# Optimization experiments

Measured on AMD Instinct MI355X. Metric: run time of the kernel, lower is better.

## Reference

```python
import jax, jax.numpy as jnp
import numpy as np

RANK = 16
ALPHA = 16.0
IN_F = 4096
OUT_F = 11008
TOKENS = 64


def setup_inputs() -> dict:
    key = jax.random.key(0)
    k_x, k_w, k_s, k_a, k_b, k_bias = jax.random.split(key, 6)
    return {
        "x": jax.random.normal(k_x, (TOKENS, IN_F), dtype=jnp.float32),
        "weight_int4": jax.random.normal(k_w, (OUT_F, IN_F), dtype=jnp.float32),
        "weight_scale": jax.random.uniform(k_s, (OUT_F,), dtype=jnp.float32),
        "lora_A": jax.random.normal(k_a, (RANK, IN_F), dtype=jnp.float32) * 0.01,
        "lora_B": jax.random.normal(k_b, (OUT_F, RANK), dtype=jnp.float32),
        "bias": jax.random.normal(k_bias, (OUT_F,), dtype=jnp.float32),
    }


def reference(x, weight_int4, weight_scale, lora_A, lora_B, bias):
    # Dequantize: per-output-channel scale.  [out, in]
    weight = weight_int4 * weight_scale[:, None]
    # LoRA delta: B @ A scaled by alpha/rank.  [out, in]
    lora_weight = (lora_B @ lora_A) * (ALPHA / RANK)
    effective_weight = weight + lora_weight
    # F.linear: x @ W^T + b  ->  [tokens, out]
    return x @ effective_weight.T + bias
```

## Files before the change

### kernel.cpp

```cpp
#include <hip/hip_runtime.h>
#include <hip/hip_bf16.h>
#include <cstdint>

#define TOK   64
#define INF   4096
#define OUTF  11008
#define KCHUNKS 128
#define QCNT  8
#define NCHB  172

using bf16x8  = __attribute__((ext_vector_type(8))) __bf16;
using floatx4 = __attribute__((ext_vector_type(4))) float;

union B8u { uint32_t u[4]; uint4 q; bf16x8 v; };

__device__ __forceinline__ uint32_t hi2(float a, float b) {
    return (__float_as_uint(a) >> 16) | (__float_as_uint(b) & 0xffff0000u);
}
__device__ __forceinline__ float losub(float x) {
    return x - __uint_as_float(__float_as_uint(x) & 0xffff0000u);
}
__device__ __forceinline__ void packW(float4 a, float4 b, B8u& wh, B8u& wl) {
    wh.u[0] = hi2(a.x, a.y);  wh.u[1] = hi2(a.z, a.w);
    wh.u[2] = hi2(b.x, b.y);  wh.u[3] = hi2(b.z, b.w);
    wl.u[0] = hi2(losub(a.x), losub(a.y));
    wl.u[1] = hi2(losub(a.z), losub(a.w));
    wl.u[2] = hi2(losub(b.x), losub(b.y));
    wl.u[3] = hi2(losub(b.z), losub(b.w));
}

__global__ __launch_bounds__(256) void k_prep(const float* __restrict__ x,
        const float* __restrict__ A,
        unsigned short* __restrict__ xh, unsigned short* __restrict__ xl,
        float* __restrict__ tm) {
    int b = blockIdx.x;
    if (b < 1024) {
        int idx  = b * 256 + threadIdx.x;
        int j    = idx & 7;
        int lane = (idx >> 3) & 63;
        int kc   = (idx >> 9) & 127;
        int mt   = idx >> 16;
        int row  = mt * 16 + (lane & 15);
        int col  = kc * 32 + ((lane >> 4) << 3) + j;
        float v  = x[(size_t)row * INF + col];
        float lo = losub(v);
        xh[idx] = (unsigned short)(__float_as_uint(v) >> 16);
        xl[idx] = (unsigned short)(__float_as_uint(lo) >> 16);
    } else {
        int bb   = b - 1024;
        int t    = bb & 63;
        int wv   = threadIdx.x >> 6, lane = threadIdx.x & 63;
        int r    = (bb >> 6) * 4 + wv;
        const float4* xr = (const float4*)(x + (size_t)t * INF);
        const float4* ar = (const float4*)(A + (size_t)r * INF);
        float s = 0.f;
#pragma unroll
        for (int i = 0; i < INF / 4 / 64; ++i) {
            float4 a = xr[lane + i * 64], c = ar[lane + i * 64];
            s += a.x * c.x + a.y * c.y + a.z * c.z + a.w * c.w;
        }
#pragma unroll
        for (int off = 32; off > 0; off >>= 1) s += __shfl_down(s, off);
        if (lane == 0) tm[t * 16 + r] = s;
    }
}

template<bool ATOMIC>
__global__ __launch_bounds__(256, 2) void k_main(const float* __restrict__ W,
        const uint4* __restrict__ xh, const uint4* __restrict__ xl,
        const float* __restrict__ scale, float* __restrict__ part,
        float* __restrict__ out) {
    __shared__ uint4 wlds[2][1024];
    __shared__ uint4 xsl [2][1024];

    int tid  = threadIdx.x;
    int lane = tid & 63;
    int wv   = tid >> 6;
    int quad = lane >> 4;
    int nb   = blockIdx.x % NCHB;
    int q    = blockIdx.x / NCHB;
    int chl  = wv * 16 + (lane & 15);
    int ch   = nb * 64 + chl;

    const int kbase = q * 512;
    int rr = lane >> 4;
    int gg = lane & 15;

    floatx4 acc[4] = {};

    auto stage = [&](int p, int bsel) {
#pragma unroll
        for (int t = 0; t < 4; ++t) {
            int i = wv * 4 + t;
            int r = i * 4 + rr;
            int f = (gg - r) & 15;
            const float* src = W + (size_t)(nb * 64 + r) * INF
                             + kbase + p * 64 + f * 4;
            __builtin_amdgcn_global_load_lds(
                (const __attribute__((address_space(1))) uint32_t*)src,
                (__attribute__((address_space(3))) uint32_t*)&wlds[bsel][i * 64],
                16, 0, 0);
        }
#pragma unroll
        for (int t = 0; t < 4; ++t) {
            int j  = wv * 4 + t;
            int hl = j >> 3, mt = (j >> 1) & 3, kc = j & 1;
            const uint4* src = (hl ? xl : xh)
                + ((size_t)(mt * KCHUNKS + q * 16 + p * 2 + kc) * 64 + lane);
            __builtin_amdgcn_global_load_lds(
                (const __attribute__((address_space(1))) uint32_t*)src,
                (__attribute__((address_space(3))) uint32_t*)&xsl[bsel][j * 64],
                16, 0, 0);
        }
    };

    stage(0, 0);
    int cur = 0;
#pragma unroll
    for (int p = 0; p < 8; ++p) {
        __syncthreads();
        if (p < 7) stage(p + 1, cur ^ 1);

#pragma unroll
        for (int kc = 0; kc < 2; ++kc) {
            int f0 = kc * 8 + quad * 2;
            uint4 wf0 = wlds[cur][chl * 16 + ((f0     + chl) & 15)];
            uint4 wf1 = wlds[cur][chl * 16 + ((f0 + 1 + chl) & 15)];
            B8u wh, wl;
            packW(*(float4*)&wf0, *(float4*)&wf1, wh, wl);
#pragma unroll
            for (int mt = 0; mt < 4; ++mt) {
                B8u ah, al;
                ah.q = xsl[cur][(    mt * 2 + kc) * 64 + lane];
                al.q = xsl[cur][(8 + mt * 2 + kc) * 64 + lane];
                acc[mt] = __builtin_amdgcn_mfma_f32_16x16x32_bf16(ah.v, wh.v, acc[mt], 0, 0, 0);
                acc[mt] = __builtin_amdgcn_mfma_f32_16x16x32_bf16(ah.v, wl.v, acc[mt], 0, 0, 0);
                acc[mt] = __builtin_amdgcn_mfma_f32_16x16x32_bf16(al.v, wh.v, acc[mt], 0, 0, 0);
            }
        }
        cur ^= 1;
    }

#pragma unroll
    for (int mt = 0; mt < 4; ++mt) {
        int token = mt * 16 + quad * 4;
#pragma unroll
        for (int r = 0; r < 4; ++r) {
            if constexpr (ATOMIC) {
                atomicAdd(&out[(size_t)(token + r) * OUTF + ch], scale[ch] * acc[mt][r]);
            } else {
                part[((size_t)q * TOK + token + r) * OUTF + ch] = acc[mt][r];
            }
        }
    }
}

__global__ __launch_bounds__(256) void k_post(const float* __restrict__ part,
        const float* __restrict__ scale, const float* __restrict__ bias,
        const float* __restrict__ lB, const float* __restrict__ tm,
        float* __restrict__ out) {
    int o = blockIdx.x * 256 + threadIdx.x;
    int t = blockIdx.y;
    if (o >= OUTF) return;
    float s = 0.f;
#pragma unroll
    for (int qq = 0; qq < QCNT; ++qq)
        s += part[((size_t)qq * TOK + t) * OUTF + o];
    const float4* Br = (const float4*)(lB + (size_t)o * 16);
    const float4* tr = (const float4*)(tm + (size_t)t * 16);
    float l = 0.f;
#pragma unroll
    for (int i = 0; i < 4; ++i) {
        float4 b = Br[i], tt = tr[i];
        l += b.x * tt.x + b.y * tt.y + b.z * tt.z + b.w * tt.w;
    }
    out[(size_t)t * OUTF + o] = s * scale[o] + l + bias[o];
}

__global__ __launch_bounds__(256) void k_pre(const float* __restrict__ bias,
        const float* __restrict__ lB, const float* __restrict__ tm,
        float* __restrict__ out) {
    int o = blockIdx.x * 256 + threadIdx.x;
    int t = blockIdx.y;
    if (o >= OUTF) return;
    const float4* Br = (const float4*)(lB + (size_t)o * 16);
    const float4* tr = (const float4*)(tm + (size_t)t * 16);
    float l = 0.f;
#pragma unroll
    for (int i = 0; i < 4; ++i) {
        float4 b = Br[i], tt = tr[i];
        l += b.x * tt.x + b.y * tt.y + b.z * tt.z + b.w * tt.w;
    }
    out[(size_t)t * OUTF + o] = l + bias[o];
}

extern "C" void kernel_launch(void* const* d_in, const int* in_sizes, int n_in,
                              void* d_out, int out_size, void* d_ws, size_t ws_size,
                              hipStream_t stream) {
    const float* x     = (const float*)d_in[0];
    const float* W     = (const float*)d_in[1];
    const float* scale = (const float*)d_in[2];
    const float* lA    = (const float*)d_in[3];
    const float* lB    = (const float*)d_in[4];
    const float* bias  = (const float*)d_in[5];
    float* out = (float*)d_out;

    char* ws = (char*)d_ws;
    unsigned short* xh = (unsigned short*)(ws);
    unsigned short* xl = (unsigned short*)(ws + 524288);
    float* tm   = (float*)(ws + 1048576);
    float* part = (float*)(ws + 1052672);
    const size_t need = 1052672 + (size_t)QCNT * TOK * OUTF * 4;

    k_prep<<<1280, 256, 0, stream>>>(x, lA, xh, xl, tm);

    if (ws_size >= need) {
        k_main<false><<<NCHB * QCNT, 256, 0, stream>>>(W, (const uint4*)xh,
                (const uint4*)xl, scale, part, out);
        k_post<<<dim3(43, TOK), 256, 0, stream>>>(part, scale, bias, lB, tm, out);
    } else {
        k_pre<<<dim3(43, TOK), 256, 0, stream>>>(bias, lB, tm, out);
        k_main<true><<<NCHB * QCNT, 256, 0, stream>>>(W, (const uint4*)xh,
                (const uint4*)xl, scale, nullptr, out);
    }
}
```

Measured before the change: 280.8 us.

## Deepen K-loop pipeline to a 4-stage LDS ring with explicit vmcnt waits

Replaces the two-buffer, 64-wide K staging with a four-buffer ring of 32-wide K slices, keeping three stages of global-to-LDS loads in flight. Each iteration waits on vmcnt only for the oldest stage and then uses a raw s_barrier instead of __syncthreads. The goal is to hide more of the global-memory latency of streaming the fp32 weights. Total LDS use is unchanged. The trade-offs are smaller tiles, more barriers per block and hand-tuned waitcnt values that depend on how many loads each stage issues.

```diff
diff --git a/kernel.cpp b/kernel.cpp
--- a/kernel.cpp
+++ b/kernel.cpp
@@ -70,8 +70,8 @@
         const uint4* __restrict__ xh, const uint4* __restrict__ xl,
         const float* __restrict__ scale, float* __restrict__ part,
         float* __restrict__ out) {
-    __shared__ uint4 wlds[2][1024];
-    __shared__ uint4 xsl [2][1024];
+    __shared__ uint4 wlds[4][512];
+    __shared__ uint4 xsl [4][512];
 
     int tid  = threadIdx.x;
     int lane = tid & 63;
@@ -83,30 +83,30 @@
     int ch   = nb * 64 + chl;
 
     const int kbase = q * 512;
-    int rr = lane >> 4;
-    int gg = lane & 15;
+    int rsub = lane >> 3;
+    int gg   = lane & 7;
 
     floatx4 acc[4] = {};
 
     auto stage = [&](int p, int bsel) {
 #pragma unroll
-        for (int t = 0; t < 4; ++t) {
-            int i = wv * 4 + t;
-            int r = i * 4 + rr;
-            int f = (gg - r) & 15;
+        for (int t = 0; t < 2; ++t) {
+            int i = wv * 2 + t;
+            int r = i * 8 + rsub;
+            int f = (gg - r) & 7;
             const float* src = W + (size_t)(nb * 64 + r) * INF
-                             + kbase + p * 64 + f * 4;
+                             + kbase + p * 32 + f * 4;
             __builtin_amdgcn_global_load_lds(
                 (const __attribute__((address_space(1))) uint32_t*)src,
                 (__attribute__((address_space(3))) uint32_t*)&wlds[bsel][i * 64],
                 16, 0, 0);
         }
 #pragma unroll
-        for (int t = 0; t < 4; ++t) {
-            int j  = wv * 4 + t;
-            int hl = j >> 3, mt = (j >> 1) & 3, kc = j & 1;
+        for (int t = 0; t < 2; ++t) {
+            int j  = wv * 2 + t;
+            int hl = j >> 2, mt = j & 3;
             const uint4* src = (hl ? xl : xh)
-                + ((size_t)(mt * KCHUNKS + q * 16 + p * 2 + kc) * 64 + lane);
+                + ((size_t)(mt * KCHUNKS + q * 16 + p) * 64 + lane);
             __builtin_amdgcn_global_load_lds(
                 (const __attribute__((address_space(1))) uint32_t*)src,
                 (__attribute__((address_space(3))) uint32_t*)&xsl[bsel][j * 64],
@@ -115,30 +115,31 @@
     };
 
     stage(0, 0);
-    int cur = 0;
-#pragma unroll
-    for (int p = 0; p < 8; ++p) {
-        __syncthreads();
-        if (p < 7) stage(p + 1, cur ^ 1);
-
-#pragma unroll
-        for (int kc = 0; kc < 2; ++kc) {
-            int f0 = kc * 8 + quad * 2;
-            uint4 wf0 = wlds[cur][chl * 16 + ((f0     + chl) & 15)];
-            uint4 wf1 = wlds[cur][chl * 16 + ((f0 + 1 + chl) & 15)];
-            B8u wh, wl;
-            packW(*(float4*)&wf0, *(float4*)&wf1, wh, wl);
-#pragma unroll
-            for (int mt = 0; mt < 4; ++mt) {
-                B8u ah, al;
-                ah.q = xsl[cur][(    mt * 2 + kc) * 64 + lane];
-                al.q = xsl[cur][(8 + mt * 2 + kc) * 64 + lane];
-                acc[mt] = __builtin_amdgcn_mfma_f32_16x16x32_bf16(ah.v, wh.v, acc[mt], 0, 0, 0);
-                acc[mt] = __builtin_amdgcn_mfma_f32_16x16x32_bf16(ah.v, wl.v, acc[mt], 0, 0, 0);
-                acc[mt] = __builtin_amdgcn_mfma_f32_16x16x32_bf16(al.v, wh.v, acc[mt], 0, 0, 0);
-            }
-        }
-        cur ^= 1;
+    stage(1, 1);
+    stage(2, 2);
+
+#pragma unroll
+    for (int p = 0; p < 16; ++p) {
+        if (p < 14)       asm volatile("s_waitcnt vmcnt(8)" ::: "memory");
+        else if (p == 14) asm volatile("s_waitcnt vmcnt(4)" ::: "memory");
+        else              asm volatile("s_waitcnt vmcnt(0)" ::: "memory");
+        __builtin_amdgcn_s_barrier();
+        if (p < 13) stage(p + 3, (p + 3) & 3);
+
+        const int buf = p & 3;
+        uint4 wf0 = wlds[buf][chl * 8 + ((quad * 2     + chl) & 7)];
+        uint4 wf1 = wlds[buf][chl * 8 + ((quad * 2 + 1 + chl) & 7)];
+        B8u wh, wl;
+        packW(*(float4*)&wf0, *(float4*)&wf1, wh, wl);
+#pragma unroll
+        for (int mt = 0; mt < 4; ++mt) {
+            B8u ah, al;
+            ah.q = xsl[buf][(    mt) * 64 + lane];
+            al.q = xsl[buf][(4 + mt) * 64 + lane];
+            acc[mt] = __builtin_amdgcn_mfma_f32_16x16x32_bf16(ah.v, wh.v, acc[mt], 0, 0, 0);
+            acc[mt] = __builtin_amdgcn_mfma_f32_16x16x32_bf16(ah.v, wl.v, acc[mt], 0, 0, 0);
+            acc[mt] = __builtin_amdgcn_mfma_f32_16x16x32_bf16(al.v, wh.v, acc[mt], 0, 0, 0);
+        }
     }
 
 #pragma unroll
```

Result: slower. 286.5 us (+2.0%).
